# Kernel tuning notes

Measured on AMD Instinct MI355X. Metric: run time of the kernel, lower is better.

Reference implementation:

```python
import jax, jax.numpy as jnp
import numpy as np

B, S, D, E, F, K = 2, 4096, 1024, 8, 2048, 2


def setup_inputs() -> dict:
    key = jax.random.key(0)
    k1, k2, k3, k4 = jax.random.split(key, 4)
    return {
        "inputs_raw": jax.random.normal(k1, (B, S, D), dtype=jnp.float32),
        "gate_w": jax.random.normal(k2, (D, E), dtype=jnp.float32) * (D ** -0.5),
        "w1": jax.random.normal(k3, (E, D, F), dtype=jnp.float32) * (D ** -0.5),
        "w2": jax.random.normal(k4, (E, F, D), dtype=jnp.float32) * (F ** -0.5),
        "top_k": K,
    }


def reference(inputs_raw, gate_w, w1, w2, top_k):
    ishape = inputs_raw.shape
    x = inputs_raw.reshape(-1, ishape[-1])                 # [T, D]
    n_experts = gate_w.shape[-1]

    # --- gating: top-k logits, softmax over the selected k (float32, like the torch code) ---
    logits = x @ gate_w                                    # [T, E]
    top_vals, top_idx = jax.lax.top_k(logits, top_k)       # [T, K]
    top_w = jax.nn.softmax(top_vals.astype(jnp.float32), axis=-1).astype(x.dtype)
    # dense combine weights [T, E]; zero for unselected experts
    combine = jnp.einsum("tk,tke->te", top_w,
                         jax.nn.one_hot(top_idx, n_experts, dtype=x.dtype))

    # --- experts: D -> F (SiLU) -> D, evaluated densely and combined with gate weights ---
    h = jax.nn.silu(jnp.einsum("td,edf->etf", x, w1))      # [E, T, F]
    y = jnp.einsum("etf,efd->etd", h, w2)                  # [E, T, D]
    out = jnp.einsum("te,etd->td", combine, y)             # [T, D]
    return out.reshape(ishape)
```

## Files before the change

kernel.cpp:

```cpp
#include <hip/hip_runtime.h>
#include <cstdint>
#include <cstddef>

#define T_TOK 8192
#define DIM   1024
#define NE    8
#define FF    2048
#define TOPK  2

typedef __bf16 bf16x8 __attribute__((ext_vector_type(8)));
typedef float  floatx4 __attribute__((ext_vector_type(4)));

__device__ __forceinline__ unsigned short f2bf(float f) {
  unsigned int u = __float_as_uint(f);
  unsigned int r = 0x7FFFu + ((u >> 16) & 1u);
  return (unsigned short)((u + r) >> 16);
}

__device__ __forceinline__ void gl_lds16(const void* g, void* l) {
  __builtin_amdgcn_global_load_lds(
      (__attribute__((address_space(1))) void*)g,
      (__attribute__((address_space(3))) void*)l,
      16, 0, 0);
}

__global__ __launch_bounds__(256) void transpose_bf16_kernel(
    const float* __restrict__ in, unsigned short* __restrict__ out,
    int R, int C)
{
  __shared__ float tile[32][33];
  int e  = blockIdx.z;
  int c0 = blockIdx.x * 32, r0 = blockIdx.y * 32;
  int tx = threadIdx.x & 31, ty = threadIdx.x >> 5;
  const float* inp = in + (size_t)e * R * C;
  unsigned short* op = out + (size_t)e * R * C;
  for (int i = 0; i < 4; ++i)
    tile[ty + i * 8][tx] = inp[(size_t)(r0 + ty + i * 8) * C + c0 + tx];
  __syncthreads();
  for (int i = 0; i < 4; ++i)
    op[(size_t)(c0 + ty + i * 8) * R + r0 + tx] = f2bf(tile[tx][ty + i * 8]);
}

__global__ __launch_bounds__(256) void gate_kernel(
    const float* __restrict__ x, const float* __restrict__ gw,
    unsigned short* __restrict__ xb, int* __restrict__ tokExp,
    float* __restrict__ tokW, int* __restrict__ cnt)
{
  __shared__ float gwT[NE][DIM];
  int tid = threadIdx.x;
  if (blockIdx.x == 0 && tid < NE) cnt[tid] = 0;
  for (int i = tid; i < DIM * NE; i += 256) {
    int d = i >> 3, e = i & 7;
    gwT[e][d] = gw[i];
  }
  __syncthreads();

  int wv = tid >> 6, lane = tid & 63;
  int t = blockIdx.x * 4 + wv;
  const float* xrow = x + (size_t)t * DIM;
  unsigned short* xbrow = xb + (size_t)t * DIM;

  double acc[NE];
  for (int e = 0; e < NE; ++e) acc[e] = 0.0;

  for (int j = 0; j < 4; ++j) {
    float4 xv = ((const float4*)xrow)[j * 64 + lane];
    ushort4 s;
    s.x = f2bf(xv.x); s.y = f2bf(xv.y); s.z = f2bf(xv.z); s.w = f2bf(xv.w);
    ((ushort4*)xbrow)[j * 64 + lane] = s;
    double xd0 = (double)xv.x, xd1 = (double)xv.y;
    double xd2 = (double)xv.z, xd3 = (double)xv.w;
    for (int e = 0; e < NE; ++e) {
      float4 g = ((const float4*)&gwT[e][0])[j * 64 + lane];
      acc[e] += xd0 * (double)g.x + xd1 * (double)g.y +
                xd2 * (double)g.z + xd3 * (double)g.w;
    }
  }

  for (int s = 32; s > 0; s >>= 1)
    for (int e = 0; e < NE; ++e)
      acc[e] += __shfl_down(acc[e], s, 64);

  if (lane == 0) {
    int e0 = 0; double v0 = acc[0];
    for (int e = 1; e < NE; ++e) if (acc[e] > v0) { v0 = acc[e]; e0 = e; }
    int e1 = -1; double v1 = -1.0e300;
    for (int e = 0; e < NE; ++e) {
      if (e == e0) continue;
      if (acc[e] > v1) { v1 = acc[e]; e1 = e; }
    }
    float a = (float)v0, b = (float)v1;
    float eb = __expf(b - a);
    float den = 1.0f + eb;
    tokExp[t] = e0 | (e1 << 8);
    tokW[2 * t + 0] = 1.0f / den;
    tokW[2 * t + 1] = eb / den;
  }
}

__global__ __launch_bounds__(256) void assign_kernel(
    const int* __restrict__ tokExp, int* __restrict__ tokEnc,
    int* __restrict__ tIdx, int* __restrict__ cnt)
{
  int t = blockIdx.x * 256 + threadIdx.x;
  int lane = threadIdx.x & 63;
  unsigned long long below = (1ull << lane) - 1ull;
  int enc = tokExp[t];
  int e0 = enc & 0xFF, e1 = (enc >> 8) & 0xFF;
  int s0 = 0, s1 = 0;
  for (int e = 0; e < NE; ++e) {
    unsigned long long m0 = __ballot(e0 == e);
    unsigned long long m1 = __ballot(e1 == e);
    int c0 = __popcll(m0), c1 = __popcll(m1);
    int base = 0;
    if (lane == 0 && (c0 + c1) > 0)
      base = atomicAdd(&cnt[e], c0 + c1);
    base = __shfl(base, 0, 64);
    if (e0 == e) s0 = base + __popcll(m0 & below);
    if (e1 == e) s1 = base + c0 + __popcll(m1 & below);
  }
  tokEnc[2 * t + 0] = (e0 << 16) | s0;
  tokEnc[2 * t + 1] = (e1 << 16) | s1;
  tIdx[e0 * T_TOK + s0] = t;
  tIdx[e1 * T_TOK + s1] = t;
}

__global__ __launch_bounds__(256, 2) void gemm1_kernel(
    const unsigned short* __restrict__ xb,
    const unsigned short* __restrict__ w1t,
    unsigned short* __restrict__ h,
    const int* __restrict__ tIdx, const int* __restrict__ cnt)
{
  int g = blockIdx.x;
  int e = g & 7;
  int b = g >> 3;
  int phase = b >> 9;
  int m = (b >> 3) & 63;
  int nl = b & 7;
  int count = cnt[e];
  int r0 = m * 128;
  if (r0 >= count) return;
  int n0 = (phase * 8 + nl) * 128;

  __shared__ __align__(16) unsigned short As[2][8][128][8];
  __shared__ __align__(16) unsigned short Bs[2][8][128][8];

  int tid = threadIdx.x, lane = tid & 63, w = tid >> 6;
  int wr = w >> 1, wc = w & 1;
  int quad = lane >> 4, li = lane & 15;

  const unsigned short* ag[2];
  const unsigned short* bg[2];
  for (int c = 0; c < 2; ++c) {
    int mm = c * 64 + lane;
    int r = r0 + mm; if (r > count - 1) r = count - 1;
    ag[c] = xb + (size_t)tIdx[e * T_TOK + r] * DIM;
    bg[c] = w1t + ((size_t)e * FF + (n0 + mm)) * DIM;
  }

  floatx4 acc[4][4];
  for (int mi = 0; mi < 4; ++mi)
    for (int ni = 0; ni < 4; ++ni)
      for (int q = 0; q < 4; ++q) acc[mi][ni][q] = 0.0f;

  auto stage = [&](int buf, int k0) {
    for (int kk = 0; kk < 2; ++kk) {
      int kq = w + kk * 4;
      gl_lds16(ag[0] + k0 + kq * 8, &As[buf][kq][0][0]);
      gl_lds16(ag[1] + k0 + kq * 8, &As[buf][kq][64][0]);
      gl_lds16(bg[0] + k0 + kq * 8, &Bs[buf][kq][0][0]);
      gl_lds16(bg[1] + k0 + kq * 8, &Bs[buf][kq][64][0]);
    }
  };

  stage(0, 0);
  __syncthreads();
  int cur = 0;
  for (int k0 = 0; k0 < DIM; k0 += 64) {
    if (k0 + 64 < DIM) stage(cur ^ 1, k0 + 64);
    for (int ks = 0; ks < 2; ++ks) {
      bf16x8 af[4], bf[4];
      for (int mi = 0; mi < 4; ++mi)
        af[mi] = *(const bf16x8*)&As[cur][ks * 4 + quad][wr * 64 + mi * 16 + li][0];
      for (int ni = 0; ni < 4; ++ni)
        bf[ni] = *(const bf16x8*)&Bs[cur][ks * 4 + quad][wc * 64 + ni * 16 + li][0];
      for (int mi = 0; mi < 4; ++mi)
        for (int ni = 0; ni < 4; ++ni)
          acc[mi][ni] = __builtin_amdgcn_mfma_f32_16x16x32_bf16(
              af[mi], bf[ni], acc[mi][ni], 0, 0, 0);
    }
    __syncthreads();
    cur ^= 1;
  }

  size_t hb = 0;
  for (int i = 0; i < e; ++i) hb += cnt[i];
  for (int mi = 0; mi < 4; ++mi) {
    int rowb = wr * 64 + mi * 16 + quad * 4;
    for (int rr = 0; rr < 4; ++rr) {
      int r = r0 + rowb + rr;
      if (r >= count) continue;
      unsigned short* hrow = h + (hb + r) * FF + n0 + wc * 64 + li;
      for (int ni = 0; ni < 4; ++ni) {
        float v = acc[mi][ni][rr];
        float s = v / (1.0f + __expf(-v));
        hrow[ni * 16] = f2bf(s);
      }
    }
  }
}

__global__ __launch_bounds__(256, 2) void gemm2_kernel(
    const unsigned short* __restrict__ h,
    const unsigned short* __restrict__ w2t,
    float* __restrict__ yv,
    const int* __restrict__ cnt)
{
  int g = blockIdx.x;
  int e = g & 7;
  int b = g >> 3;
  int phase = b >> 8;
  int m = (b >> 2) & 63;
  int nl = b & 3;
  int count = cnt[e];
  int r0 = m * 128;
  if (r0 >= count) return;
  int n0 = (phase * 4 + nl) * 128;

  __shared__ __align__(16) unsigned short As[2][8][128][8];
  __shared__ __align__(16) unsigned short Bs[2][8][128][8];

  int tid = threadIdx.x, lane = tid & 63, w = tid >> 6;
  int wr = w >> 1, wc = w & 1;
  int quad = lane >> 4, li = lane & 15;
  size_t yb = 0;
  for (int i = 0; i < e; ++i) yb += cnt[i];

  const unsigned short* ag[2];
  const unsigned short* bg[2];
  for (int c = 0; c < 2; ++c) {
    int mm = c * 64 + lane;
    int r = r0 + mm; if (r > count - 1) r = count - 1;
    ag[c] = h + (yb + r) * FF;
    bg[c] = w2t + ((size_t)e * DIM + (n0 + mm)) * FF;
  }

  floatx4 acc[4][4];
  for (int mi = 0; mi < 4; ++mi)
    for (int ni = 0; ni < 4; ++ni)
      for (int q = 0; q < 4; ++q) acc[mi][ni][q] = 0.0f;

  auto stage = [&](int buf, int k0) {
    for (int kk = 0; kk < 2; ++kk) {
      int kq = w + kk * 4;
      gl_lds16(ag[0] + k0 + kq * 8, &As[buf][kq][0][0]);
      gl_lds16(ag[1] + k0 + kq * 8, &As[buf][kq][64][0]);
      gl_lds16(bg[0] + k0 + kq * 8, &Bs[buf][kq][0][0]);
      gl_lds16(bg[1] + k0 + kq * 8, &Bs[buf][kq][64][0]);
    }
  };

  stage(0, 0);
  __syncthreads();
  int cur = 0;
  for (int k0 = 0; k0 < FF; k0 += 64) {
    if (k0 + 64 < FF) stage(cur ^ 1, k0 + 64);
    for (int ks = 0; ks < 2; ++ks) {
      bf16x8 af[4], bf[4];
      for (int mi = 0; mi < 4; ++mi)
        af[mi] = *(const bf16x8*)&As[cur][ks * 4 + quad][wr * 64 + mi * 16 + li][0];
      for (int ni = 0; ni < 4; ++ni)
        bf[ni] = *(const bf16x8*)&Bs[cur][ks * 4 + quad][wc * 64 + ni * 16 + li][0];
      for (int mi = 0; mi < 4; ++mi)
        for (int ni = 0; ni < 4; ++ni)
          acc[mi][ni] = __builtin_amdgcn_mfma_f32_16x16x32_bf16(
              af[mi], bf[ni], acc[mi][ni], 0, 0, 0);
    }
    __syncthreads();
    cur ^= 1;
  }

  for (int mi = 0; mi < 4; ++mi) {
    int rowb = wr * 64 + mi * 16 + quad * 4;
    for (int rr = 0; rr < 4; ++rr) {
      int r = r0 + rowb + rr;
      if (r >= count) continue;
      float* yrow = yv + (yb + r) * DIM + n0 + wc * 64 + li;
      for (int ni = 0; ni < 4; ++ni)
        yrow[ni * 16] = acc[mi][ni][rr];
    }
  }
}

__global__ __launch_bounds__(256) void combine_kernel(
    const float* __restrict__ yv, const int* __restrict__ tokEnc,
    const float* __restrict__ tokW, const int* __restrict__ cnt,
    float* __restrict__ out)
{
  int t = blockIdx.x;
  int i = threadIdx.x;
  int enc0 = tokEnc[2 * t + 0], enc1 = tokEnc[2 * t + 1];
  float w0 = tokW[2 * t + 0], w1 = tokW[2 * t + 1];
  int x0 = enc0 >> 16, x1 = enc1 >> 16;
  int off0 = 0, off1 = 0, a = 0;
  for (int e = 0; e < NE; ++e) {
    if (e == x0) off0 = a;
    if (e == x1) off1 = a;
    a += cnt[e];
  }
  size_t row0 = (size_t)off0 + (enc0 & 0xFFFF);
  size_t row1 = (size_t)off1 + (enc1 & 0xFFFF);
  float4 va = ((const float4*)(yv + row0 * DIM))[i];
  float4 vb = ((const float4*)(yv + row1 * DIM))[i];
  float4 o;
  o.x = w0 * va.x + w1 * vb.x;
  o.y = w0 * va.y + w1 * vb.y;
  o.z = w0 * va.z + w1 * vb.z;
  o.w = w0 * va.w + w1 * vb.w;
  ((float4*)(out + (size_t)t * DIM))[i] = o;
}

extern "C" void kernel_launch(void* const* d_in, const int* in_sizes, int n_in,
                              void* d_out, int out_size, void* d_ws, size_t ws_size,
                              hipStream_t stream)
{
  const float* x  = (const float*)d_in[0];
  const float* gw = (const float*)d_in[1];
  const float* w1 = (const float*)d_in[2];
  const float* w2 = (const float*)d_in[3];
  float* out = (float*)d_out;

  size_t o = 0;
  auto alloc = [&](size_t bytes) {
    void* p = (char*)d_ws + o;
    o += (bytes + 255) & ~(size_t)255;
    return p;
  };
  unsigned short* xb   = (unsigned short*)alloc((size_t)T_TOK * DIM * 2);
  unsigned short* w1t  = (unsigned short*)alloc((size_t)NE * DIM * FF * 2);
  unsigned short* w2t  = (unsigned short*)alloc((size_t)NE * DIM * FF * 2);
  unsigned short* hbuf = (unsigned short*)alloc((size_t)T_TOK * TOPK * FF * 2);
  float*          yv   = (float*)alloc((size_t)T_TOK * TOPK * DIM * 4);
  int*   tIdx   = (int*)alloc((size_t)NE * T_TOK * 4);
  int*   tokEnc = (int*)alloc((size_t)2 * T_TOK * 4);
  float* tokW   = (float*)alloc((size_t)2 * T_TOK * 4);
  int*   tokExp = (int*)alloc((size_t)T_TOK * 4);
  int*   cnt    = (int*)alloc((size_t)NE * 4);

  transpose_bf16_kernel<<<dim3(FF / 32, DIM / 32, NE), 256, 0, stream>>>(w1, w1t, DIM, FF);
  transpose_bf16_kernel<<<dim3(DIM / 32, FF / 32, NE), 256, 0, stream>>>(w2, w2t, FF, DIM);

  gate_kernel<<<T_TOK / 4, 256, 0, stream>>>(x, gw, xb, tokExp, tokW, cnt);
  assign_kernel<<<T_TOK / 256, 256, 0, stream>>>(tokExp, tokEnc, tIdx, cnt);

  gemm1_kernel<<<8192, 256, 0, stream>>>(xb, w1t, hbuf, tIdx, cnt);
  gemm2_kernel<<<4096, 256, 0, stream>>>(hbuf, w2t, yv, cnt);
  combine_kernel<<<T_TOK, 256, 0, stream>>>(yv, tokEnc, tokW, cnt, out);
}
```

Measured before the change: 584.3 us.

## Use 256x256 tiles with 8 waves and interleaved load/MFMA pipeline for expert GEMMs

After: 620.1 us. 1.06x slower.

```diff
diff --git a/kernel.cpp b/kernel.cpp
--- a/kernel.cpp
+++ b/kernel.cpp
@@ -125,7 +125,106 @@
   tIdx[e1 * T_TOK + s1] = t;
 }
 
-__global__ __launch_bounds__(256, 2) void gemm1_kernel(
+template<int KDIM>
+__device__ __forceinline__ void mfma_core(
+    const unsigned short* (&agp)[4], const unsigned short* (&bgp)[4],
+    unsigned short* smem, floatx4 (&acc)[8][4])
+{
+  constexpr int NKT = KDIM / 64;
+  const int tid = threadIdx.x, lane = tid & 63, w = tid >> 6;
+  const int wm = w >> 2, wn = w & 3;
+  const int quad = lane >> 4, li = lane & 15;
+
+  unsigned short (*As)[8][256][8] = (unsigned short (*)[8][256][8])smem;
+  unsigned short (*Bs)[8][256][8] = (unsigned short (*)[8][256][8])(smem + 32768);
+
+  #define STAGE_A(BUF, KT, HALF) do { \
+    gl_lds16(agp[(HALF)*2+0] + (KT)*64 + w*8, &As[BUF][w][(HALF)*128 +  0][0]); \
+    gl_lds16(agp[(HALF)*2+1] + (KT)*64 + w*8, &As[BUF][w][(HALF)*128 + 64][0]); } while(0)
+  #define STAGE_B(BUF, KT, HALF) do { \
+    gl_lds16(bgp[(HALF)*2+0] + (KT)*64 + w*8, &Bs[BUF][w][(HALF)*128 +  0][0]); \
+    gl_lds16(bgp[(HALF)*2+1] + (KT)*64 + w*8, &Bs[BUF][w][(HALF)*128 + 64][0]); } while(0)
+
+  STAGE_B(0, 0, 0); STAGE_B(0, 0, 1);
+  STAGE_A(0, 0, 0); STAGE_A(0, 0, 1);
+  STAGE_B(1, 1, 0); STAGE_B(1, 1, 1);
+
+  for (int t0 = 0; t0 < NKT; t0 += 2) {
+    bf16x8 bf[4][2];
+    #pragma unroll
+    for (int q = 0; q < 4; ++q) {
+      if (q == 0) STAGE_A(1, t0 + 1, 0);
+      if (q == 1) { STAGE_A(1, t0 + 1, 1); if (t0 + 2 < NKT) STAGE_B(0, t0 + 2, 0); }
+      if (q == 2) { if (t0 + 2 < NKT) STAGE_B(0, t0 + 2, 1); }
+      if (q == 0) asm volatile("s_waitcnt vmcnt(6)" ::: "memory");
+      asm volatile("s_barrier" ::: "memory");
+      if (q == 0) {
+        #pragma unroll
+        for (int ni = 0; ni < 4; ++ni)
+          #pragma unroll
+          for (int kk = 0; kk < 2; ++kk)
+            bf[ni][kk] = *(const bf16x8*)&Bs[0][kk * 4 + quad][wn * 64 + ni * 16 + li][0];
+      }
+      bf16x8 af[2][2];
+      #pragma unroll
+      for (int j = 0; j < 2; ++j)
+        #pragma unroll
+        for (int kk = 0; kk < 2; ++kk)
+          af[j][kk] = *(const bf16x8*)&As[0][kk * 4 + quad][wm * 128 + (2 * q + j) * 16 + li][0];
+      __builtin_amdgcn_s_setprio(1);
+      #pragma unroll
+      for (int j = 0; j < 2; ++j)
+        #pragma unroll
+        for (int ni = 0; ni < 4; ++ni)
+          #pragma unroll
+          for (int kk = 0; kk < 2; ++kk)
+            acc[2 * q + j][ni] = __builtin_amdgcn_mfma_f32_16x16x32_bf16(
+                af[j][kk], bf[ni][kk], acc[2 * q + j][ni], 0, 0, 0);
+      __builtin_amdgcn_s_setprio(0);
+      asm volatile("s_barrier" ::: "memory");
+    }
+    #pragma unroll
+    for (int q = 0; q < 4; ++q) {
+      if (q == 0) { if (t0 + 2 < NKT) STAGE_A(0, t0 + 2, 0); }
+      if (q == 1) { if (t0 + 2 < NKT) STAGE_A(0, t0 + 2, 1); }
+      if (q == 2) { if (t0 + 3 < NKT) STAGE_B(1, t0 + 3, 0); }
+      if (q == 3) { if (t0 + 3 < NKT) STAGE_B(1, t0 + 3, 1); }
+      if (q == 0) {
+        if (t0 + 2 < NKT) asm volatile("s_waitcnt vmcnt(6)" ::: "memory");
+        else              asm volatile("s_waitcnt vmcnt(0)" ::: "memory");
+      }
+      asm volatile("s_barrier" ::: "memory");
+      if (q == 0) {
+        #pragma unroll
+        for (int ni = 0; ni < 4; ++ni)
+          #pragma unroll
+          for (int kk = 0; kk < 2; ++kk)
+            bf[ni][kk] = *(const bf16x8*)&Bs[1][kk * 4 + quad][wn * 64 + ni * 16 + li][0];
+      }
+      bf16x8 af[2][2];
+      #pragma unroll
+      for (int j = 0; j < 2; ++j)
+        #pragma unroll
+        for (int kk = 0; kk < 2; ++kk)
+          af[j][kk] = *(const bf16x8*)&As[1][kk * 4 + quad][wm * 128 + (2 * q + j) * 16 + li][0];
+      __builtin_amdgcn_s_setprio(1);
+      #pragma unroll
+      for (int j = 0; j < 2; ++j)
+        #pragma unroll
+        for (int ni = 0; ni < 4; ++ni)
+          #pragma unroll
+          for (int kk = 0; kk < 2; ++kk)
+            acc[2 * q + j][ni] = __builtin_amdgcn_mfma_f32_16x16x32_bf16(
+                af[j][kk], bf[ni][kk], acc[2 * q + j][ni], 0, 0, 0);
+      __builtin_amdgcn_s_setprio(0);
+      asm volatile("s_barrier" ::: "memory");
+    }
+  }
+  #undef STAGE_A
+  #undef STAGE_B
+}
+
+__global__ __launch_bounds__(512, 2) void gemm1_kernel(
     const unsigned short* __restrict__ xb,
     const unsigned short* __restrict__ w1t,
     unsigned short* __restrict__ h,
@@ -134,73 +233,44 @@
   int g = blockIdx.x;
   int e = g & 7;
   int b = g >> 3;
-  int phase = b >> 9;
-  int m = (b >> 3) & 63;
-  int nl = b & 7;
+  int m = b & 31;
+  int n = b >> 5;
   int count = cnt[e];
-  int r0 = m * 128;
+  int r0 = m * 256;
   if (r0 >= count) return;
-  int n0 = (phase * 8 + nl) * 128;
-
-  __shared__ __align__(16) unsigned short As[2][8][128][8];
-  __shared__ __align__(16) unsigned short Bs[2][8][128][8];
-
-  int tid = threadIdx.x, lane = tid & 63, w = tid >> 6;
-  int wr = w >> 1, wc = w & 1;
-  int quad = lane >> 4, li = lane & 15;
-
-  const unsigned short* ag[2];
-  const unsigned short* bg[2];
-  for (int c = 0; c < 2; ++c) {
-    int mm = c * 64 + lane;
-    int r = r0 + mm; if (r > count - 1) r = count - 1;
-    ag[c] = xb + (size_t)tIdx[e * T_TOK + r] * DIM;
-    bg[c] = w1t + ((size_t)e * FF + (n0 + mm)) * DIM;
-  }
-
-  floatx4 acc[4][4];
-  for (int mi = 0; mi < 4; ++mi)
+  int n0 = n * 256;
+
+  __shared__ __align__(16) unsigned short smem[2 * 8 * 256 * 8 * 2];
+
+  int tid = threadIdx.x, lane = tid & 63;
+  const unsigned short* agp[4];
+  const unsigned short* bgp[4];
+  #pragma unroll
+  for (int gq = 0; gq < 4; ++gq) {
+    int r = r0 + gq * 64 + lane; if (r > count - 1) r = count - 1;
+    agp[gq] = xb + (size_t)tIdx[e * T_TOK + r] * DIM;
+    bgp[gq] = w1t + ((size_t)e * FF + (n0 + gq * 64 + lane)) * DIM;
+  }
+
+  floatx4 acc[8][4];
+  #pragma unroll
+  for (int mi = 0; mi < 8; ++mi)
+    #pragma unroll
     for (int ni = 0; ni < 4; ++ni)
-      for (int q = 0; q < 4; ++q) acc[mi][ni][q] = 0.0f;
-
-  auto stage = [&](int buf, int k0) {
-    for (int kk = 0; kk < 2; ++kk) {
-      int kq = w + kk * 4;
-      gl_lds16(ag[0] + k0 + kq * 8, &As[buf][kq][0][0]);
-      gl_lds16(ag[1] + k0 + kq * 8, &As[buf][kq][64][0]);
-      gl_lds16(bg[0] + k0 + kq * 8, &Bs[buf][kq][0][0]);
-      gl_lds16(bg[1] + k0 + kq * 8, &Bs[buf][kq][64][0]);
-    }
-  };
-
-  stage(0, 0);
-  __syncthreads();
-  int cur = 0;
-  for (int k0 = 0; k0 < DIM; k0 += 64) {
-    if (k0 + 64 < DIM) stage(cur ^ 1, k0 + 64);
-    for (int ks = 0; ks < 2; ++ks) {
-      bf16x8 af[4], bf[4];
-      for (int mi = 0; mi < 4; ++mi)
-        af[mi] = *(const bf16x8*)&As[cur][ks * 4 + quad][wr * 64 + mi * 16 + li][0];
-      for (int ni = 0; ni < 4; ++ni)
-        bf[ni] = *(const bf16x8*)&Bs[cur][ks * 4 + quad][wc * 64 + ni * 16 + li][0];
-      for (int mi = 0; mi < 4; ++mi)
-        for (int ni = 0; ni < 4; ++ni)
-          acc[mi][ni] = __builtin_amdgcn_mfma_f32_16x16x32_bf16(
-              af[mi], bf[ni], acc[mi][ni], 0, 0, 0);
-    }
-    __syncthreads();
-    cur ^= 1;
-  }
+      #pragma unroll
+      for (int qq = 0; qq < 4; ++qq) acc[mi][ni][qq] = 0.0f;
+
+  mfma_core<DIM>(agp, bgp, smem, acc);
 
   size_t hb = 0;
   for (int i = 0; i < e; ++i) hb += cnt[i];
-  for (int mi = 0; mi < 4; ++mi) {
-    int rowb = wr * 64 + mi * 16 + quad * 4;
+  int w = tid >> 6, wm = w >> 2, wn = w & 3, quad = lane >> 4, li = lane & 15;
+  for (int mi = 0; mi < 8; ++mi) {
+    int rowb = wm * 128 + mi * 16 + quad * 4;
     for (int rr = 0; rr < 4; ++rr) {
       int r = r0 + rowb + rr;
       if (r >= count) continue;
-      unsigned short* hrow = h + (hb + r) * FF + n0 + wc * 64 + li;
+      unsigned short* hrow = h + (hb + r) * FF + n0 + wn * 64 + li;
       for (int ni = 0; ni < 4; ++ni) {
         float v = acc[mi][ni][rr];
         float s = v / (1.0f + __expf(-v));
@@ -210,7 +280,7 @@
   }
 }
 
-__global__ __launch_bounds__(256, 2) void gemm2_kernel(
+__global__ __launch_bounds__(512, 2) void gemm2_kernel(
     const unsigned short* __restrict__ h,
     const unsigned short* __restrict__ w2t,
     float* __restrict__ yv,
@@ -219,73 +289,45 @@
   int g = blockIdx.x;
   int e = g & 7;
   int b = g >> 3;
-  int phase = b >> 8;
-  int m = (b >> 2) & 63;
-  int nl = b & 3;
+  int m = b & 31;
+  int n = b >> 5;
   int count = cnt[e];
-  int r0 = m * 128;
+  int r0 = m * 256;
   if (r0 >= count) return;
-  int n0 = (phase * 4 + nl) * 128;
-
-  __shared__ __align__(16) unsigned short As[2][8][128][8];
-  __shared__ __align__(16) unsigned short Bs[2][8][128][8];
-
-  int tid = threadIdx.x, lane = tid & 63, w = tid >> 6;
-  int wr = w >> 1, wc = w & 1;
-  int quad = lane >> 4, li = lane & 15;
+  int n0 = n * 256;
+
+  __shared__ __align__(16) unsigned short smem[2 * 8 * 256 * 8 * 2];
+
+  int tid = threadIdx.x, lane = tid & 63;
   size_t yb = 0;
   for (int i = 0; i < e; ++i) yb += cnt[i];
 
-  const unsigned short* ag[2];
-  const unsigned short* bg[2];
-  for (int c = 0; c < 2; ++c) {
-    int mm = c * 64 + lane;
-    int r = r0 + mm; if (r > count - 1) r = count - 1;
-    ag[c] = h + (yb + r) * FF;
-    bg[c] = w2t + ((size_t)e * DIM + (n0 + mm)) * FF;
-  }
-
-  floatx4 acc[4][4];
-  for (int mi = 0; mi < 4; ++mi)
+  const unsigned short* agp[4];
+  const unsigned short* bgp[4];
+  #pragma unroll
+  for (int gq = 0; gq < 4; ++gq) {
+    int r = r0 + gq * 64 + lane; if (r > count - 1) r = count - 1;
+    agp[gq] = h + (yb + r) * FF;
+    bgp[gq] = w2t + ((size_t)e * DIM + (n0 + gq * 64 + lane)) * FF;
+  }
+
+  floatx4 acc[8][4];
+  #pragma unroll
+  for (int mi = 0; mi < 8; ++mi)
+    #pragma unroll
     for (int ni = 0; ni < 4; ++ni)
-      for (int q = 0; q < 4; ++q) acc[mi][ni][q] = 0.0f;
-
-  auto stage = [&](int buf, int k0) {
-    for (int kk = 0; kk < 2; ++kk) {
-      int kq = w + kk * 4;
-      gl_lds16(ag[0] + k0 + kq * 8, &As[buf][kq][0][0]);
-      gl_lds16(ag[1] + k0 + kq * 8, &As[buf][kq][64][0]);
-      gl_lds16(bg[0] + k0 + kq * 8, &Bs[buf][kq][0][0]);
-      gl_lds16(bg[1] + k0 + kq * 8, &Bs[buf][kq][64][0]);
-    }
-  };
-
-  stage(0, 0);
-  __syncthreads();
-  int cur = 0;
-  for (int k0 = 0; k0 < FF; k0 += 64) {
-    if (k0 + 64 < FF) stage(cur ^ 1, k0 + 64);
-    for (int ks = 0; ks < 2; ++ks) {
-      bf16x8 af[4], bf[4];
-      for (int mi = 0; mi < 4; ++mi)
-        af[mi] = *(const bf16x8*)&As[cur][ks * 4 + quad][wr * 64 + mi * 16 + li][0];
-      for (int ni = 0; ni < 4; ++ni)
-        bf[ni] = *(const bf16x8*)&Bs[cur][ks * 4 + quad][wc * 64 + ni * 16 + li][0];
-      for (int mi = 0; mi < 4; ++mi)
-        for (int ni = 0; ni < 4; ++ni)
-          acc[mi][ni] = __builtin_amdgcn_mfma_f32_16x16x32_bf16(
-              af[mi], bf[ni], acc[mi][ni], 0, 0, 0);
-    }
-    __syncthreads();
-    cur ^= 1;
-  }
-
-  for (int mi = 0; mi < 4; ++mi) {
-    int rowb = wr * 64 + mi * 16 + quad * 4;
+      #pragma unroll
+      for (int qq = 0; qq < 4; ++qq) acc[mi][ni][qq] = 0.0f;
+
+  mfma_core<FF>(agp, bgp, smem, acc);
+
+  int w = tid >> 6, wm = w >> 2, wn = w & 3, quad = lane >> 4, li = lane & 15;
+  for (int mi = 0; mi < 8; ++mi) {
+    int rowb = wm * 128 + mi * 16 + quad * 4;
     for (int rr = 0; rr < 4; ++rr) {
       int r = r0 + rowb + rr;
       if (r >= count) continue;
-      float* yrow = yv + (yb + r) * DIM + n0 + wc * 64 + li;
+      float* yrow = yv + (yb + r) * DIM + n0 + wn * 64 + li;
       for (int ni = 0; ni < 4; ++ni)
         yrow[ni * 16] = acc[mi][ni][rr];
     }
@@ -353,7 +395,7 @@
   gate_kernel<<<T_TOK / 4, 256, 0, stream>>>(x, gw, xb, tokExp, tokW, cnt);
   assign_kernel<<<T_TOK / 256, 256, 0, stream>>>(tokExp, tokEnc, tIdx, cnt);
 
-  gemm1_kernel<<<8192, 256, 0, stream>>>(xb, w1t, hbuf, tIdx, cnt);
-  gemm2_kernel<<<4096, 256, 0, stream>>>(hbuf, w2t, yv, cnt);
+  gemm1_kernel<<<NE * 8 * 32, 512, 0, stream>>>(xb, w1t, hbuf, tIdx, cnt);
+  gemm2_kernel<<<NE * 4 * 32, 512, 0, stream>>>(hbuf, w2t, yv, cnt);
   combine_kernel<<<T_TOK, 256, 0, stream>>>(yv, tokEnc, tokW, cnt, out);
 }
```

## Single-buffer GEMM LDS tiles for higher occupancy and merge weight transposes

Applied to the files above, without the earlier changes.

New measurement: 544.7 us. 6.8% less time.

```diff
diff --git a/kernel.cpp b/kernel.cpp
--- a/kernel.cpp
+++ b/kernel.cpp
@@ -24,16 +24,21 @@
       16, 0, 0);
 }
 
-__global__ __launch_bounds__(256) void transpose_bf16_kernel(
-    const float* __restrict__ in, unsigned short* __restrict__ out,
-    int R, int C)
+__global__ __launch_bounds__(256) void transpose2_bf16_kernel(
+    const float* __restrict__ w1, unsigned short* __restrict__ w1t,
+    const float* __restrict__ w2, unsigned short* __restrict__ w2t)
 {
   __shared__ float tile[32][33];
-  int e  = blockIdx.z;
-  int c0 = blockIdx.x * 32, r0 = blockIdx.y * 32;
+  int z = blockIdx.z;
+  int e = z & 7, sel = z >> 3;
+  int R = sel ? FF : DIM;
+  int C = sel ? DIM : FF;
+  const float* inp = (sel ? w2 : w1) + (size_t)e * R * C;
+  unsigned short* op = (sel ? w2t : w1t) + (size_t)e * R * C;
+  int nc = C >> 5;
+  int bx = blockIdx.x;
+  int c0 = (bx % nc) * 32, r0 = (bx / nc) * 32;
   int tx = threadIdx.x & 31, ty = threadIdx.x >> 5;
-  const float* inp = in + (size_t)e * R * C;
-  unsigned short* op = out + (size_t)e * R * C;
   for (int i = 0; i < 4; ++i)
     tile[ty + i * 8][tx] = inp[(size_t)(r0 + ty + i * 8) * C + c0 + tx];
   __syncthreads();
@@ -125,7 +130,7 @@
   tIdx[e1 * T_TOK + s1] = t;
 }
 
-__global__ __launch_bounds__(256, 2) void gemm1_kernel(
+__global__ __launch_bounds__(256, 4) void gemm1_kernel(
     const unsigned short* __restrict__ xb,
     const unsigned short* __restrict__ w1t,
     unsigned short* __restrict__ h,
@@ -142,8 +147,8 @@
   if (r0 >= count) return;
   int n0 = (phase * 8 + nl) * 128;
 
-  __shared__ __align__(16) unsigned short As[2][8][128][8];
-  __shared__ __align__(16) unsigned short Bs[2][8][128][8];
+  __shared__ __align__(16) unsigned short As[8][128][8];
+  __shared__ __align__(16) unsigned short Bs[8][128][8];
 
   int tid = threadIdx.x, lane = tid & 63, w = tid >> 6;
   int wr = w >> 1, wc = w & 1;
@@ -163,34 +168,27 @@
     for (int ni = 0; ni < 4; ++ni)
       for (int q = 0; q < 4; ++q) acc[mi][ni][q] = 0.0f;
 
-  auto stage = [&](int buf, int k0) {
+  for (int k0 = 0; k0 < DIM; k0 += 64) {
+    __syncthreads();
     for (int kk = 0; kk < 2; ++kk) {
       int kq = w + kk * 4;
-      gl_lds16(ag[0] + k0 + kq * 8, &As[buf][kq][0][0]);
-      gl_lds16(ag[1] + k0 + kq * 8, &As[buf][kq][64][0]);
-      gl_lds16(bg[0] + k0 + kq * 8, &Bs[buf][kq][0][0]);
-      gl_lds16(bg[1] + k0 + kq * 8, &Bs[buf][kq][64][0]);
-    }
-  };
-
-  stage(0, 0);
-  __syncthreads();
-  int cur = 0;
-  for (int k0 = 0; k0 < DIM; k0 += 64) {
-    if (k0 + 64 < DIM) stage(cur ^ 1, k0 + 64);
+      gl_lds16(ag[0] + k0 + kq * 8, &As[kq][0][0]);
+      gl_lds16(ag[1] + k0 + kq * 8, &As[kq][64][0]);
+      gl_lds16(bg[0] + k0 + kq * 8, &Bs[kq][0][0]);
+      gl_lds16(bg[1] + k0 + kq * 8, &Bs[kq][64][0]);
+    }
+    __syncthreads();
     for (int ks = 0; ks < 2; ++ks) {
       bf16x8 af[4], bf[4];
       for (int mi = 0; mi < 4; ++mi)
-        af[mi] = *(const bf16x8*)&As[cur][ks * 4 + quad][wr * 64 + mi * 16 + li][0];
+        af[mi] = *(const bf16x8*)&As[ks * 4 + quad][wr * 64 + mi * 16 + li][0];
       for (int ni = 0; ni < 4; ++ni)
-        bf[ni] = *(const bf16x8*)&Bs[cur][ks * 4 + quad][wc * 64 + ni * 16 + li][0];
+        bf[ni] = *(const bf16x8*)&Bs[ks * 4 + quad][wc * 64 + ni * 16 + li][0];
       for (int mi = 0; mi < 4; ++mi)
         for (int ni = 0; ni < 4; ++ni)
           acc[mi][ni] = __builtin_amdgcn_mfma_f32_16x16x32_bf16(
               af[mi], bf[ni], acc[mi][ni], 0, 0, 0);
     }
-    __syncthreads();
-    cur ^= 1;
   }
 
   size_t hb = 0;
@@ -210,7 +208,7 @@
   }
 }
 
-__global__ __launch_bounds__(256, 2) void gemm2_kernel(
+__global__ __launch_bounds__(256, 4) void gemm2_kernel(
     const unsigned short* __restrict__ h,
     const unsigned short* __restrict__ w2t,
     float* __restrict__ yv,
@@ -227,8 +225,8 @@
   if (r0 >= count) return;
   int n0 = (phase * 4 + nl) * 128;
 
-  __shared__ __align__(16) unsigned short As[2][8][128][8];
-  __shared__ __align__(16) unsigned short Bs[2][8][128][8];
+  __shared__ __align__(16) unsigned short As[8][128][8];
+  __shared__ __align__(16) unsigned short Bs[8][128][8];
 
   int tid = threadIdx.x, lane = tid & 63, w = tid >> 6;
   int wr = w >> 1, wc = w & 1;
@@ -250,34 +248,27 @@
     for (int ni = 0; ni < 4; ++ni)
       for (int q = 0; q < 4; ++q) acc[mi][ni][q] = 0.0f;
 
-  auto stage = [&](int buf, int k0) {
+  for (int k0 = 0; k0 < FF; k0 += 64) {
+    __syncthreads();
     for (int kk = 0; kk < 2; ++kk) {
       int kq = w + kk * 4;
-      gl_lds16(ag[0] + k0 + kq * 8, &As[buf][kq][0][0]);
-      gl_lds16(ag[1] + k0 + kq * 8, &As[buf][kq][64][0]);
-      gl_lds16(bg[0] + k0 + kq * 8, &Bs[buf][kq][0][0]);
-      gl_lds16(bg[1] + k0 + kq * 8, &Bs[buf][kq][64][0]);
-    }
-  };
-
-  stage(0, 0);
-  __syncthreads();
-  int cur = 0;
-  for (int k0 = 0; k0 < FF; k0 += 64) {
-    if (k0 + 64 < FF) stage(cur ^ 1, k0 + 64);
+      gl_lds16(ag[0] + k0 + kq * 8, &As[kq][0][0]);
+      gl_lds16(ag[1] + k0 + kq * 8, &As[kq][64][0]);
+      gl_lds16(bg[0] + k0 + kq * 8, &Bs[kq][0][0]);
+      gl_lds16(bg[1] + k0 + kq * 8, &Bs[kq][64][0]);
+    }
+    __syncthreads();
     for (int ks = 0; ks < 2; ++ks) {
       bf16x8 af[4], bf[4];
       for (int mi = 0; mi < 4; ++mi)
-        af[mi] = *(const bf16x8*)&As[cur][ks * 4 + quad][wr * 64 + mi * 16 + li][0];
+        af[mi] = *(const bf16x8*)&As[ks * 4 + quad][wr * 64 + mi * 16 + li][0];
       for (int ni = 0; ni < 4; ++ni)
-        bf[ni] = *(const bf16x8*)&Bs[cur][ks * 4 + quad][wc * 64 + ni * 16 + li][0];
+        bf[ni] = *(const bf16x8*)&Bs[ks * 4 + quad][wc * 64 + ni * 16 + li][0];
       for (int mi = 0; mi < 4; ++mi)
         for (int ni = 0; ni < 4; ++ni)
           acc[mi][ni] = __builtin_amdgcn_mfma_f32_16x16x32_bf16(
               af[mi], bf[ni], acc[mi][ni], 0, 0, 0);
     }
-    __syncthreads();
-    cur ^= 1;
   }
 
   for (int mi = 0; mi < 4; ++mi) {
@@ -347,8 +338,7 @@
   int*   tokExp = (int*)alloc((size_t)T_TOK * 4);
   int*   cnt    = (int*)alloc((size_t)NE * 4);
 
-  transpose_bf16_kernel<<<dim3(FF / 32, DIM / 32, NE), 256, 0, stream>>>(w1, w1t, DIM, FF);
-  transpose_bf16_kernel<<<dim3(DIM / 32, FF / 32, NE), 256, 0, stream>>>(w2, w2t, FF, DIM);
+  transpose2_bf16_kernel<<<dim3(2048, 1, 2 * NE), 256, 0, stream>>>(w1, w1t, w2, w2t);
 
   gate_kernel<<<T_TOK / 4, 256, 0, stream>>>(x, gw, xb, tokExp, tokW, cnt);
   assign_kernel<<<T_TOK / 256, 256, 0, stream>>>(tokExp, tokEnc, tIdx, cnt);
```
